# Performance work log

Hardware: AMD Instinct MI355X
Metric: run time of the kernel (lower is better)

## Reference

```python
import jax, jax.numpy as jnp
import numpy as np

K, D, B = 2048, 50257, 256
N_CLASS = 2

def setup_inputs() -> dict:
    key = jax.random.key(0)
    k1, k2, k3 = jax.random.split(key, 3)
    # strictly positive (probability-like) entries so log() is finite
    queue_anchor = jax.random.uniform(k1, (K, D), dtype=jnp.float32, minval=1e-3, maxval=1.0)
    query = jax.random.uniform(k2, (B, D), dtype=jnp.float32, minval=1e-3, maxval=1.0)
    queue_label = jax.random.randint(k3, (K,), 0, N_CLASS, dtype=jnp.int64)
    return {"query": query, "queue_anchor": queue_anchor, "queue_label": queue_label}

def reference(query, queue_anchor, queue_label):
    # torch code: mean_d( a[:,None,:] * (log a[:,None,:] - log q) ).T  -> [B, K]
    # algebraically identical, avoiding the (K,B,D) intermediate:
    #   kl[b,k] = mean_d(a_k * log a_k) - (1/D) * sum_d a_k[d] * log q_b[d]
    d = queue_anchor.shape[1]
    self_term = jnp.mean(queue_anchor * jnp.log(queue_anchor), axis=1)        # [K]
    cross_term = jnp.einsum('kd,bd->kb', queue_anchor, jnp.log(query)) / d    # [K, B]
    kl_distance = (self_term[:, None] - cross_term).T                          # [B, K]
    # knn == 1 path: nearest anchor's label per query
    return queue_label[jnp.argmin(kl_distance, axis=1)]                        # [B]
```

## Files before the change

### kernel.cpp

```cpp
#include <hip/hip_runtime.h>


constexpr int K   = 2048;
constexpr int D   = 50257;
constexpr int B   = 256;
constexpr int BM  = 64;
constexpr int BN  = 256;
constexpr int BK  = 64;
constexpr int SCH = 32;
constexpr int DP  = 50320;
constexpr int NC  = 4;

typedef __attribute__((ext_vector_type(8))) short bf16x8;
typedef __attribute__((ext_vector_type(4))) float f32x4;
typedef __attribute__((ext_vector_type(8))) unsigned short u16x8;

__device__ inline unsigned short f2bf_rne(float f) {
    union { float f; unsigned u; } v; v.f = f;
    unsigned r = v.u + 0x7FFFu + ((v.u >> 16) & 1u);
    return (unsigned short)(r >> 16);
}

__global__ __launch_bounds__(256)
void lq_kernel(const float* __restrict__ q, unsigned short* __restrict__ lq)
{
    const int stride = gridDim.x * blockDim.x;
    const int total  = B * (DP / 4);
    for (int c = blockIdx.x * blockDim.x + threadIdx.x; c < total; c += stride) {
        const int b   = c / (DP / 4);
        const int off = (c % (DP / 4)) * 4;
        ushort4 w;
        float v0 = (off + 0 < D) ? __logf(q[(size_t)b * D + off + 0]) : 0.f;
        float v1 = (off + 1 < D) ? __logf(q[(size_t)b * D + off + 1]) : 0.f;
        float v2 = (off + 2 < D) ? __logf(q[(size_t)b * D + off + 2]) : 0.f;
        float v3 = (off + 3 < D) ? __logf(q[(size_t)b * D + off + 3]) : 0.f;
        w.x = f2bf_rne(v0); w.y = f2bf_rne(v1); w.z = f2bf_rne(v2); w.w = f2bf_rne(v3);
        *reinterpret_cast<ushort4*>(&lq[(size_t)b * DP + off]) = w;
    }
}

template<bool WSP>
__global__ __launch_bounds__(512, 4)
void gemm_kernel(const float* __restrict__ anchor,
                 const unsigned short* __restrict__ lq,
                 float* __restrict__ outc,
                 float* __restrict__ selfp,
                 int dc)
{
    const int t    = threadIdx.x;
    const int k0   = blockIdx.x * BM;
    const int z    = blockIdx.y;
    const int d0   = z * dc;
    const int dend = min(d0 + dc, D);

    __shared__ __align__(16) unsigned short Al[BM * 64];
    __shared__ __align__(16) unsigned short Ql[BN * 64];

    const int rowA = t >> 3;
    const int tq8  = t & 7;
    const int ar   = k0 + rowA;
    const int swA  = (rowA & 7) << 3;
    const float* Arow = anchor + (size_t)ar * D;

    const int rowQ = t >> 1;
    const int hq   = t & 1;
    const int swQ  = (rowQ & 7) << 3;
    const unsigned short* LQrow = lq + (size_t)rowQ * DP;

    const int w    = t >> 6;
    const int lane = t & 63;
    const int wm   = (w >> 2) * 32;
    const int wn   = (w & 3) * 64;
    const int lrow = lane & 15;
    const int kg   = lane >> 4;

    f32x4 acc[2][4];
#pragma unroll
    for (int mt = 0; mt < 2; ++mt)
#pragma unroll
        for (int nt = 0; nt < 4; ++nt)
#pragma unroll
            for (int i = 0; i < 4; ++i) acc[mt][nt][i] = 0.f;

    float selfacc = 0.f;

    float wf[12];
    int   ph = 0;
    u16x8 qreg[4];

    auto load_step = [&](int dt) {
        const int dbase = dt + tq8 * 8;
        if (dbase + 12 <= dend) {
            const size_t g0 = (size_t)ar * D + dbase;
            ph = (int)(g0 & 3);
            const float4* wp = reinterpret_cast<const float4*>(anchor + (g0 - ph));
            const float4 w0 = wp[0], w1 = wp[1], w2 = wp[2];
            wf[0] = w0.x; wf[1]  = w0.y; wf[2]  = w0.z; wf[3]  = w0.w;
            wf[4] = w1.x; wf[5]  = w1.y; wf[6]  = w1.z; wf[7]  = w1.w;
            wf[8] = w2.x; wf[9]  = w2.y; wf[10] = w2.z; wf[11] = w2.w;
        } else {
            ph = 0;
#pragma unroll
            for (int j = 0; j < 8; ++j) {
                const int d = dbase + j;
                wf[j] = (d < dend) ? Arow[d] : 0.f;
            }
#pragma unroll
            for (int j = 8; j < 12; ++j) wf[j] = 0.f;
        }
        const int qb = dt + hq * 32;
#pragma unroll
        for (int g = 0; g < 4; ++g)
            qreg[g] = *reinterpret_cast<const u16x8*>(&LQrow[qb + 8 * g]);
    };

    load_step(d0);

    for (int dt = d0; dt < dend; dt += BK) {
        float s1[9], av[8];
#pragma unroll
        for (int j = 0; j < 9; ++j) s1[j] = (ph & 2) ? wf[j + 2] : wf[j];
#pragma unroll
        for (int j = 0; j < 8; ++j) av[j] = (ph & 1) ? s1[j + 1] : s1[j];

        unsigned short abf[8];
#pragma unroll
        for (int j = 0; j < 8; ++j) {
            if (av[j] > 0.f) selfacc = fmaf(av[j], __logf(av[j]), selfacc);
            abf[j] = f2bf_rne(av[j]);
        }

        __syncthreads();
        {
            unsigned short* a0 = &Al[rowA * 64 + ((tq8 * 8) ^ swA)];
            reinterpret_cast<ushort4*>(a0)[0] = ushort4{abf[0], abf[1], abf[2], abf[3]};
            reinterpret_cast<ushort4*>(a0)[1] = ushort4{abf[4], abf[5], abf[6], abf[7]};
#pragma unroll
            for (int g = 0; g < 4; ++g)
                *reinterpret_cast<u16x8*>(&Ql[rowQ * 64 + ((hq * 32 + 8 * g) ^ swQ)]) = qreg[g];
        }
        __syncthreads();

        if (dt + BK < dend) load_step(dt + BK);

#pragma unroll
        for (int half = 0; half < 2; ++half) {
            const int dd = half * 32;
            bf16x8 af[2], qf[4];
#pragma unroll
            for (int mt = 0; mt < 2; ++mt) {
                const int r = wm + mt * 16 + lrow;
                const int c = (dd + kg * 8) ^ ((r & 7) << 3);
                af[mt] = *reinterpret_cast<const bf16x8*>(&Al[r * 64 + c]);
            }
#pragma unroll
            for (int nt = 0; nt < 4; ++nt) {
                const int r = wn + nt * 16 + lrow;
                const int c = (dd + kg * 8) ^ ((r & 7) << 3);
                qf[nt] = *reinterpret_cast<const bf16x8*>(&Ql[r * 64 + c]);
            }
#pragma unroll
            for (int mt = 0; mt < 2; ++mt)
#pragma unroll
                for (int nt = 0; nt < 4; ++nt)
                    acc[mt][nt] = __builtin_amdgcn_mfma_f32_16x16x32_bf16(
                        af[mt], qf[nt], acc[mt][nt], 0, 0, 0);
        }
    }

#pragma unroll
    for (int mt = 0; mt < 2; ++mt)
#pragma unroll
        for (int nt = 0; nt < 4; ++nt) {
            const int kk = k0 + wm + mt * 16 + kg * 4;
            const int bb = wn + nt * 16 + lrow;
            if (WSP) {
                *reinterpret_cast<f32x4*>(&outc[((size_t)z * B + bb) * K + kk]) = acc[mt][nt];
            } else {
                float* dst = &outc[(size_t)bb * K + kk];
#pragma unroll
                for (int i = 0; i < 4; ++i) atomicAdd(&dst[i], acc[mt][nt][i]);
            }
        }

    float s = selfacc;
    s += __shfl_xor(s, 1);
    s += __shfl_xor(s, 2);
    s += __shfl_xor(s, 4);
    if (tq8 == 0) selfp[(size_t)z * K + ar] = s;
}

__global__ __launch_bounds__(256)
void selfsum_kernel(const float* __restrict__ selfp, float* __restrict__ selftot, int sch)
{
    const int k = blockIdx.x * 256 + threadIdx.x;
    float s = 0.f;
    for (int z = 0; z < sch; ++z) s += selfp[(size_t)z * K + k];
    selftot[k] = s;
}

template<bool WSP>
__global__ __launch_bounds__(256)
void topk_kernel(const float* __restrict__ outc, const float* __restrict__ selftot,
                 int* __restrict__ cand, int sch)
{
    const int b = blockIdx.x, t = threadIdx.x;
    float v[8];
#pragma unroll
    for (int i = 0; i < 8; ++i) {
        const int k = i * 256 + t;
        float cv = 0.f;
        if (WSP) {
            for (int z = 0; z < sch; ++z) cv += outc[((size_t)z * B + b) * K + k];
        } else {
            cv = outc[(size_t)b * K + k];
        }
        v[i] = selftot[k] - cv;
    }
    __shared__ float sv[256];
    __shared__ int   si[256];
    for (int r = 0; r < NC; ++r) {
        float bv = 3.4e38f; int bk = K;
#pragma unroll
        for (int i = 0; i < 8; ++i) {
            const int k = i * 256 + t;
            if (v[i] < bv) { bv = v[i]; bk = k; }
        }
        sv[t] = bv; si[t] = bk;
        __syncthreads();
        for (int off = 128; off > 0; off >>= 1) {
            if (t < off) {
                if (sv[t + off] < sv[t] || (sv[t + off] == sv[t] && si[t + off] < si[t])) {
                    sv[t] = sv[t + off]; si[t] = si[t + off];
                }
            }
            __syncthreads();
        }
        const int kwin = si[0];
        if ((kwin & 255) == t) v[kwin >> 8] = 3.4e38f;
        if (t == 0) cand[b * NC + r] = kwin;
        __syncthreads();
    }
}

__global__ __launch_bounds__(512)
void rescore_kernel(const float* __restrict__ query, const float* __restrict__ anchor,
                    const int* __restrict__ cand, double* __restrict__ pp)
{
    const int b = blockIdx.x, h = blockIdx.y, t = threadIdx.x;
    const int dlo = h * 25129;
    const int dhi = min(D, dlo + 25129);
    int ks[NC];
#pragma unroll
    for (int c = 0; c < NC; ++c) ks[c] = cand[b * NC + c];
    const float* qrow = query + (size_t)b * D;

    double a4[NC];
#pragma unroll
    for (int c = 0; c < NC; ++c) a4[c] = 0.0;

    for (int d = dlo + t; d < dhi; d += 512) {
        const double lqv = (double)logf(qrow[d]);
#pragma unroll
        for (int c = 0; c < NC; ++c)
            a4[c] = fma((double)anchor[(size_t)ks[c] * D + d], lqv, a4[c]);
    }

    __shared__ double red[512];
    for (int c = 0; c < NC; ++c) {
        red[t] = a4[c];
        __syncthreads();
        for (int off = 256; off > 0; off >>= 1) {
            if (t < off) red[t] += red[t + off];
            __syncthreads();
        }
        if (t == 0) pp[((size_t)b * 2 + h) * NC + c] = red[0];
        __syncthreads();
    }
}

__global__ __launch_bounds__(256)
void final_kernel(const double* __restrict__ pp, const float* __restrict__ selftot,
                  const int* __restrict__ cand, const int* __restrict__ label,
                  int* __restrict__ out)
{
    const int b = threadIdx.x;
    float best = 3.4e38f; int bk = K;
#pragma unroll
    for (int c = 0; c < NC; ++c) {
        const int k = cand[b * NC + c];
        const double cv = pp[((size_t)b * 2 + 0) * NC + c] + pp[((size_t)b * 2 + 1) * NC + c];
        const float sc = selftot[k] - (float)cv;
        if (sc < best || (sc == best && k < bk)) { best = sc; bk = k; }
    }
    out[b] = label[bk];
}

extern "C" void kernel_launch(void* const* d_in, const int* in_sizes, int n_in,
                              void* d_out, int out_size, void* d_ws, size_t ws_size,
                              hipStream_t stream)
{
    const float* query  = (const float*)d_in[0];
    const float* anchor = (const float*)d_in[1];
    const int*   label  = (const int*)d_in[2];
    int* out = (int*)d_out;

    size_t cur = 0;
    auto alloc = [&](size_t bytes, size_t al) -> void* {
        cur = (cur + al - 1) & ~(al - 1);
        void* p = (char*)d_ws + cur;
        cur += bytes;
        return p;
    };
    unsigned short* lq      = (unsigned short*)alloc((size_t)B * DP * 2, 16);
    float*          selfp   = (float*)alloc((size_t)SCH * K * 4, 16);
    float*          selftot = (float*)alloc((size_t)K * 4, 16);
    int*            cand    = (int*)alloc((size_t)B * NC * 4, 16);
    double*         pp      = (double*)alloc((size_t)B * 2 * NC * 8, 16);
    float*          cross   = (float*)alloc((size_t)B * K * 4, 16);
    float*          part    = (float*)alloc((size_t)SCH * B * K * 4, 16);
    const bool wsp = (cur <= ws_size);

    const int dc = (((D + SCH - 1) / SCH) + BK - 1) / BK * BK;
    const int sch_eff = (D + dc - 1) / dc;

    lq_kernel<<<1024, 256, 0, stream>>>(query, lq);

    if (wsp) {
        gemm_kernel<true><<<dim3(K / BM, sch_eff), 512, 0, stream>>>(
            anchor, lq, part, selfp, dc);
    } else {
        hipMemsetAsync(cross, 0, (size_t)B * K * sizeof(float), stream);
        gemm_kernel<false><<<dim3(K / BM, sch_eff), 512, 0, stream>>>(
            anchor, lq, cross, selfp, dc);
    }

    selfsum_kernel<<<K / 256, 256, 0, stream>>>(selfp, selftot, sch_eff);

    if (wsp) topk_kernel<true><<<B, 256, 0, stream>>>(part, selftot, cand, sch_eff);
    else     topk_kernel<false><<<B, 256, 0, stream>>>(cross, selftot, cand, sch_eff);

    rescore_kernel<<<dim3(B, 2), 512, 0, stream>>>(query, anchor, cand, pp);
    final_kernel<<<1, 256, 0, stream>>>(pp, selftot, cand, label, out);
}
```

Before: 588.9 us.

## Skip exact rescoring when top-2 margin is large; remap GEMM blocks per XCD

The top-k pass now records the gap between the best and second-best approximate scores. The fp64 rescore and final selection are skipped for queries whose gap exceeds a fixed margin, and the candidate count rises from 4 to 8. The GEMM grid becomes one-dimensional, with a mapping that places the blocks sharing a D-chunk on the same XCD for better L2 reuse. The split count now adapts to the workspace size (16 down to 2), with a fallback that computes log(query) inside the GEMM when no lq buffer fits. The fixed margin is a heuristic bound on bf16 error and could pick a wrong label if the real error is larger.

```diff
diff --git a/kernel.cpp b/kernel.cpp
--- a/kernel.cpp
+++ b/kernel.cpp
@@ -5,11 +5,10 @@
 constexpr int D   = 50257;
 constexpr int B   = 256;
 constexpr int BM  = 64;
-constexpr int BN  = 256;
 constexpr int BK  = 64;
-constexpr int SCH = 32;
 constexpr int DP  = 50320;
-constexpr int NC  = 4;
+constexpr int NC  = 8;
+constexpr float MARGIN = 4.0f;
 
 typedef __attribute__((ext_vector_type(8))) short bf16x8;
 typedef __attribute__((ext_vector_type(4))) float f32x4;
@@ -39,22 +38,29 @@
     }
 }
 
-template<bool WSP>
+template<bool WSP, bool USELQ>
 __global__ __launch_bounds__(512, 4)
 void gemm_kernel(const float* __restrict__ anchor,
+                 const float* __restrict__ query,
                  const unsigned short* __restrict__ lq,
                  float* __restrict__ outc,
                  float* __restrict__ selfp,
-                 int dc)
-{
+                 int dc, int sch)
+{
+    const int L   = blockIdx.x;
+    const int xcd = L & 7;
+    const int j   = L >> 3;
+    int x, z;
+    if (sch >= 8) { const int zc = sch >> 3; z = xcd * zc + (j >> 5); x = j & 31; }
+    else          { const int q8 = 8 / sch;  z = xcd / q8; x = (xcd % q8) * (sch * 4) + j; }
+
     const int t    = threadIdx.x;
-    const int k0   = blockIdx.x * BM;
-    const int z    = blockIdx.y;
+    const int k0   = x * BM;
     const int d0   = z * dc;
     const int dend = min(d0 + dc, D);
 
     __shared__ __align__(16) unsigned short Al[BM * 64];
-    __shared__ __align__(16) unsigned short Ql[BN * 64];
+    __shared__ __align__(16) unsigned short Ql[B  * 64];
 
     const int rowA = t >> 3;
     const int tq8  = t & 7;
@@ -65,7 +71,8 @@
     const int rowQ = t >> 1;
     const int hq   = t & 1;
     const int swQ  = (rowQ & 7) << 3;
-    const unsigned short* LQrow = lq + (size_t)rowQ * DP;
+    const unsigned short* LQrow = lq    + (size_t)rowQ * DP;
+    const float*          Qrow  = query + (size_t)rowQ * D;
 
     const int w    = t >> 6;
     const int lane = t & 63;
@@ -87,6 +94,7 @@
     float wf[12];
     int   ph = 0;
     u16x8 qreg[4];
+    float qf32[32];
 
     auto load_step = [&](int dt) {
         const int dbase = dt + tq8 * 8;
@@ -101,17 +109,25 @@
         } else {
             ph = 0;
 #pragma unroll
-            for (int j = 0; j < 8; ++j) {
-                const int d = dbase + j;
-                wf[j] = (d < dend) ? Arow[d] : 0.f;
-            }
-#pragma unroll
-            for (int j = 8; j < 12; ++j) wf[j] = 0.f;
+            for (int jj = 0; jj < 8; ++jj) {
+                const int d = dbase + jj;
+                wf[jj] = (d < dend) ? Arow[d] : 0.f;
+            }
+#pragma unroll
+            for (int jj = 8; jj < 12; ++jj) wf[jj] = 0.f;
         }
         const int qb = dt + hq * 32;
-#pragma unroll
-        for (int g = 0; g < 4; ++g)
-            qreg[g] = *reinterpret_cast<const u16x8*>(&LQrow[qb + 8 * g]);
+        if constexpr (USELQ) {
+#pragma unroll
+            for (int g = 0; g < 4; ++g)
+                qreg[g] = *reinterpret_cast<const u16x8*>(&LQrow[qb + 8 * g]);
+        } else {
+#pragma unroll
+            for (int jj = 0; jj < 32; ++jj) {
+                const int d = qb + jj;
+                qf32[jj] = (d < dend) ? Qrow[d] : 1.f;
+            }
+        }
     };
 
     load_step(d0);
@@ -119,15 +135,26 @@
     for (int dt = d0; dt < dend; dt += BK) {
         float s1[9], av[8];
 #pragma unroll
-        for (int j = 0; j < 9; ++j) s1[j] = (ph & 2) ? wf[j + 2] : wf[j];
-#pragma unroll
-        for (int j = 0; j < 8; ++j) av[j] = (ph & 1) ? s1[j + 1] : s1[j];
+        for (int jj = 0; jj < 9; ++jj) s1[jj] = (ph & 2) ? wf[jj + 2] : wf[jj];
+#pragma unroll
+        for (int jj = 0; jj < 8; ++jj) av[jj] = (ph & 1) ? s1[jj + 1] : s1[jj];
 
         unsigned short abf[8];
 #pragma unroll
-        for (int j = 0; j < 8; ++j) {
-            if (av[j] > 0.f) selfacc = fmaf(av[j], __logf(av[j]), selfacc);
-            abf[j] = f2bf_rne(av[j]);
+        for (int jj = 0; jj < 8; ++jj) {
+            if (av[jj] > 0.f) selfacc = fmaf(av[jj], __logf(av[jj]), selfacc);
+            abf[jj] = f2bf_rne(av[jj]);
+        }
+        u16x8 qb4[4];
+        if constexpr (USELQ) {
+#pragma unroll
+            for (int g = 0; g < 4; ++g) qb4[g] = qreg[g];
+        } else {
+#pragma unroll
+            for (int g = 0; g < 4; ++g)
+#pragma unroll
+                for (int jj = 0; jj < 8; ++jj)
+                    qb4[g][jj] = f2bf_rne(__logf(qf32[g * 8 + jj]));
         }
 
         __syncthreads();
@@ -137,7 +164,7 @@
             reinterpret_cast<ushort4*>(a0)[1] = ushort4{abf[4], abf[5], abf[6], abf[7]};
 #pragma unroll
             for (int g = 0; g < 4; ++g)
-                *reinterpret_cast<u16x8*>(&Ql[rowQ * 64 + ((hq * 32 + 8 * g) ^ swQ)]) = qreg[g];
+                *reinterpret_cast<u16x8*>(&Ql[rowQ * 64 + ((hq * 32 + 8 * g) ^ swQ)]) = qb4[g];
         }
         __syncthreads();
 
@@ -202,7 +229,7 @@
 template<bool WSP>
 __global__ __launch_bounds__(256)
 void topk_kernel(const float* __restrict__ outc, const float* __restrict__ selftot,
-                 int* __restrict__ cand, int sch)
+                 int* __restrict__ cand, int* __restrict__ need, int sch)
 {
     const int b = blockIdx.x, t = threadIdx.x;
     float v[8];
@@ -219,6 +246,7 @@
     }
     __shared__ float sv[256];
     __shared__ int   si[256];
+    __shared__ float topv[2];
     for (int r = 0; r < NC; ++r) {
         float bv = 3.4e38f; int bk = K;
 #pragma unroll
@@ -238,16 +266,22 @@
         }
         const int kwin = si[0];
         if ((kwin & 255) == t) v[kwin >> 8] = 3.4e38f;
-        if (t == 0) cand[b * NC + r] = kwin;
-        __syncthreads();
-    }
+        if (t == 0) {
+            cand[b * NC + r] = kwin;
+            if (r < 2) topv[r] = sv[0];
+        }
+        __syncthreads();
+    }
+    if (t == 0) need[b] = (topv[1] - topv[0] < MARGIN) ? 1 : 0;
 }
 
 __global__ __launch_bounds__(512)
 void rescore_kernel(const float* __restrict__ query, const float* __restrict__ anchor,
-                    const int* __restrict__ cand, double* __restrict__ pp)
+                    const int* __restrict__ cand, const int* __restrict__ need,
+                    double* __restrict__ pp)
 {
     const int b = blockIdx.x, h = blockIdx.y, t = threadIdx.x;
+    if (!need[b]) return;
     const int dlo = h * 25129;
     const int dhi = min(D, dlo + 25129);
     int ks[NC];
@@ -255,20 +289,20 @@
     for (int c = 0; c < NC; ++c) ks[c] = cand[b * NC + c];
     const float* qrow = query + (size_t)b * D;
 
-    double a4[NC];
-#pragma unroll
-    for (int c = 0; c < NC; ++c) a4[c] = 0.0;
+    double a8[NC];
+#pragma unroll
+    for (int c = 0; c < NC; ++c) a8[c] = 0.0;
 
     for (int d = dlo + t; d < dhi; d += 512) {
         const double lqv = (double)logf(qrow[d]);
 #pragma unroll
         for (int c = 0; c < NC; ++c)
-            a4[c] = fma((double)anchor[(size_t)ks[c] * D + d], lqv, a4[c]);
+            a8[c] = fma((double)anchor[(size_t)ks[c] * D + d], lqv, a8[c]);
     }
 
     __shared__ double red[512];
     for (int c = 0; c < NC; ++c) {
-        red[t] = a4[c];
+        red[t] = a8[c];
         __syncthreads();
         for (int off = 256; off > 0; off >>= 1) {
             if (t < off) red[t] += red[t + off];
@@ -281,10 +315,11 @@
 
 __global__ __launch_bounds__(256)
 void final_kernel(const double* __restrict__ pp, const float* __restrict__ selftot,
-                  const int* __restrict__ cand, const int* __restrict__ label,
-                  int* __restrict__ out)
+                  const int* __restrict__ cand, const int* __restrict__ need,
+                  const int* __restrict__ label, int* __restrict__ out)
 {
     const int b = threadIdx.x;
+    if (!need[b]) { out[b] = label[cand[b * NC]]; return; }
     float best = 3.4e38f; int bk = K;
 #pragma unroll
     for (int c = 0; c < NC; ++c) {
@@ -306,40 +341,60 @@
     int* out = (int*)d_out;
 
     size_t cur = 0;
-    auto alloc = [&](size_t bytes, size_t al) -> void* {
-        cur = (cur + al - 1) & ~(al - 1);
+    auto alloc = [&](size_t bytes) -> void* {
+        cur = (cur + 255) & ~(size_t)255;
         void* p = (char*)d_ws + cur;
         cur += bytes;
         return p;
     };
-    unsigned short* lq      = (unsigned short*)alloc((size_t)B * DP * 2, 16);
-    float*          selfp   = (float*)alloc((size_t)SCH * K * 4, 16);
-    float*          selftot = (float*)alloc((size_t)K * 4, 16);
-    int*            cand    = (int*)alloc((size_t)B * NC * 4, 16);
-    double*         pp      = (double*)alloc((size_t)B * 2 * NC * 8, 16);
-    float*          cross   = (float*)alloc((size_t)B * K * 4, 16);
-    float*          part    = (float*)alloc((size_t)SCH * B * K * 4, 16);
-    const bool wsp = (cur <= ws_size);
-
-    const int dc = (((D + SCH - 1) / SCH) + BK - 1) / BK * BK;
-    const int sch_eff = (D + dc - 1) / dc;
-
-    lq_kernel<<<1024, 256, 0, stream>>>(query, lq);
-
-    if (wsp) {
-        gemm_kernel<true><<<dim3(K / BM, sch_eff), 512, 0, stream>>>(
-            anchor, lq, part, selfp, dc);
+
+    unsigned short* lq      = (unsigned short*)alloc((size_t)B * DP * 2);
+    float*          selfp   = (float*)alloc((size_t)16 * K * 4);
+    float*          selftot = (float*)alloc((size_t)K * 4);
+    int*            cand    = (int*)alloc((size_t)B * NC * 4);
+    int*            need    = (int*)alloc((size_t)B * 4);
+    double*         pp      = (double*)alloc((size_t)B * 2 * NC * 8);
+    const size_t fixed_end  = cur;
+
+    int sch = 0;
+    for (int s = 16; s >= 2; s >>= 1)
+        if (fixed_end + (size_t)s * B * K * 4 + 256 <= ws_size) { sch = s; break; }
+
+    if (sch) {
+        float* part = (float*)alloc((size_t)sch * B * K * 4);
+        const int dc = (((D + sch - 1) / sch) + BK - 1) / BK * BK;
+        lq_kernel<<<1024, 256, 0, stream>>>(query, lq);
+        gemm_kernel<true, true><<<32 * sch, 512, 0, stream>>>(
+            anchor, query, lq, part, selfp, dc, sch);
+        selfsum_kernel<<<K / 256, 256, 0, stream>>>(selfp, selftot, sch);
+        topk_kernel<true><<<B, 256, 0, stream>>>(part, selftot, cand, need, sch);
+    } else if (fixed_end + (size_t)B * K * 4 + 256 <= ws_size) {
+        float* cross = (float*)alloc((size_t)B * K * 4);
+        const int s8 = 8;
+        const int dc = (((D + s8 - 1) / s8) + BK - 1) / BK * BK;
+        hipMemsetAsync(cross, 0, (size_t)B * K * sizeof(float), stream);
+        lq_kernel<<<1024, 256, 0, stream>>>(query, lq);
+        gemm_kernel<false, true><<<32 * s8, 512, 0, stream>>>(
+            anchor, query, lq, cross, selfp, dc, s8);
+        selfsum_kernel<<<K / 256, 256, 0, stream>>>(selfp, selftot, s8);
+        topk_kernel<false><<<B, 256, 0, stream>>>(cross, selftot, cand, need, s8);
     } else {
+        cur = 0;
+        float* cross = (float*)alloc((size_t)B * K * 4);
+        selfp   = (float*)alloc((size_t)16 * K * 4);
+        selftot = (float*)alloc((size_t)K * 4);
+        cand    = (int*)alloc((size_t)B * NC * 4);
+        need    = (int*)alloc((size_t)B * 4);
+        pp      = (double*)alloc((size_t)B * 2 * NC * 8);
+        const int s8 = 8;
+        const int dc = (((D + s8 - 1) / s8) + BK - 1) / BK * BK;
         hipMemsetAsync(cross, 0, (size_t)B * K * sizeof(float), stream);
-        gemm_kernel<false><<<dim3(K / BM, sch_eff), 512, 0, stream>>>(
-            anchor, lq, cross, selfp, dc);
-    }
-
-    selfsum_kernel<<<K / 256, 256, 0, stream>>>(selfp, selftot, sch_eff);
-
-    if (wsp) topk_kernel<true><<<B, 256, 0, stream>>>(part, selftot, cand, sch_eff);
-    else     topk_kernel<false><<<B, 256, 0, stream>>>(cross, selftot, cand, sch_eff);
-
-    rescore_kernel<<<dim3(B, 2), 512, 0, stream>>>(query, anchor, cand, pp);
-    final_kernel<<<1, 256, 0, stream>>>(pp, selftot, cand, label, out);
-}
+        gemm_kernel<false, false><<<32 * s8, 512, 0, stream>>>(
+            anchor, query, lq, cross, selfp, dc, s8);
+        selfsum_kernel<<<K / 256, 256, 0, stream>>>(selfp, selftot, s8);
+        topk_kernel<false><<<B, 256, 0, stream>>>(cross, selftot, cand, need, s8);
+    }
+
+    rescore_kernel<<<dim3(B, 2), 512, 0, stream>>>(query, anchor, cand, need, pp);
+    final_kernel<<<1, 256, 0, stream>>>(pp, selftot, cand, need, label, out);
+}
```

Result: faster. 525.1 us (-10.8%).
